# Optimization experiments

Hardware: AMD Instinct MI355X
Metric: run time of the kernel (lower is better)

Reference implementation:

```python
import jax, jax.numpy as jnp
import numpy as np

USER = 50000
ITEM = 20000
N = USER + ITEM
LATDIM = 64
GNN_LAYERS = 2
LAM = 0.2  # args.ris_adj_lambda
IMG_DIM = 4096
TXT_DIM = 768
E_MAIN = 2_000_000
E_MODAL = 1_000_000


def setup_inputs() -> dict:
    key = jax.random.key(0)
    ks = jax.random.split(key, 25)
    f32 = jnp.float32
    inp = {
        "image_embedding": jax.random.normal(ks[0], (ITEM, IMG_DIM), f32),
        "text_embedding": jax.random.normal(ks[1], (ITEM, TXT_DIM), f32),
        "adj_rows": jax.random.randint(ks[2], (E_MAIN,), 0, N, jnp.int32),
        "adj_cols": jax.random.randint(ks[3], (E_MAIN,), 0, N, jnp.int32),
        "adj_vals": jax.random.uniform(ks[4], (E_MAIN,), f32),
        "img_rows": jax.random.randint(ks[5], (E_MODAL,), 0, N, jnp.int32),
        "img_cols": jax.random.randint(ks[6], (E_MODAL,), 0, N, jnp.int32),
        "img_vals": jax.random.uniform(ks[7], (E_MODAL,), f32),
        "txt_rows": jax.random.randint(ks[8], (E_MODAL,), 0, N, jnp.int32),
        "txt_cols": jax.random.randint(ks[9], (E_MODAL,), 0, N, jnp.int32),
        "txt_vals": jax.random.uniform(ks[10], (E_MODAL,), f32),
        "u_sh": jax.random.normal(ks[11], (USER, LATDIM), f32) * 0.1,
        "i_sh": jax.random.normal(ks[12], (ITEM, LATDIM), f32) * 0.1,
        "Wi_sh": jax.random.normal(ks[13], (IMG_DIM, LATDIM), f32) * 0.02,
        "bi_sh": jnp.zeros((LATDIM,), f32),
        "Wt_sh": jax.random.normal(ks[14], (TXT_DIM, LATDIM), f32) * 0.02,
        "bt_sh": jnp.zeros((LATDIM,), f32),
        "u_vsp": jax.random.normal(ks[15], (USER, LATDIM), f32) * 0.1,
        "i_vsp": jax.random.normal(ks[16], (ITEM, LATDIM), f32) * 0.1,
        "Wi_vsp": jax.random.normal(ks[17], (IMG_DIM, LATDIM), f32) * 0.02,
        "bi_vsp": jnp.zeros((LATDIM,), f32),
        "u_tsp": jax.random.normal(ks[18], (USER, LATDIM), f32) * 0.1,
        "i_tsp": jax.random.normal(ks[19], (ITEM, LATDIM), f32) * 0.1,
        "Wt_tsp": jax.random.normal(ks[20], (TXT_DIM, LATDIM), f32) * 0.02,
        "bt_tsp": jnp.zeros((LATDIM,), f32),
    }
    return inp


def _spmm(rows, cols, vals, x):
    # sparse COO [N,N] @ dense [N,D]: gather source rows, scale, scatter-add to dest rows
    return jax.ops.segment_sum(vals[:, None] * x[cols], rows, num_segments=N)


def _l2norm(x):
    # F.normalize(x, p=2, dim=1), eps=1e-12
    n = jnp.linalg.norm(x, axis=1, keepdims=True)
    return x / jnp.maximum(n, 1e-12)


def _branch(uE, iE, feats, ar, ac, av, mr, mc, mv):
    base = jnp.concatenate([uE, iE], axis=0)
    e_adj = _spmm(mr, mc, mv, base)                                   # modal graph aggregation
    e = _spmm(ar, ac, av, jnp.concatenate([uE, _l2norm(feats)], 0))   # pass 1: normalized modal feats
    e2 = _spmm(ar, ac, av, jnp.concatenate([e[:USER], iE], 0))        # pass 2: propagated users + id emb
    e = e + e2 + LAM * e_adj
    total = e
    cur = e
    for _ in range(GNN_LAYERS):
        cur = _spmm(ar, ac, av, cur)
        total = total + cur
    return total  # [N, LATDIM]


def reference(image_embedding, text_embedding,
              adj_rows, adj_cols, adj_vals,
              img_rows, img_cols, img_vals,
              txt_rows, txt_cols, txt_vals,
              u_sh, i_sh, Wi_sh, bi_sh, Wt_sh, bt_sh,
              u_vsp, i_vsp, Wi_vsp, bi_vsp,
              u_tsp, i_tsp, Wt_tsp, bt_tsp):
    # trans == 1: Linear feature projections
    img_sh = image_embedding @ Wi_sh + bi_sh
    txt_sh = text_embedding @ Wt_sh + bt_sh
    # shared-modal model (Model_modal_sh.forward_MM)
    ev_sh = _branch(u_sh, i_sh, img_sh, adj_rows, adj_cols, adj_vals, img_rows, img_cols, img_vals)
    et_sh = _branch(u_sh, i_sh, txt_sh, adj_rows, adj_cols, adj_vals, txt_rows, txt_cols, txt_vals)
    sh = jnp.concatenate([ev_sh, et_sh], axis=-1)  # [N, 2*LATDIM]
    # visual-specific model (Model_visual_sp.forward_MM)
    img_sp = image_embedding @ Wi_vsp + bi_vsp
    ev_sp = _branch(u_vsp, i_vsp, img_sp, adj_rows, adj_cols, adj_vals, img_rows, img_cols, img_vals)
    # text-specific model (Model_text_sp.forward_MM)
    txt_sp = text_embedding @ Wt_tsp + bt_tsp
    et_sp = _branch(u_tsp, i_tsp, txt_sp, adj_rows, adj_cols, adj_vals, txt_rows, txt_cols, txt_vals)
    # pack all model outputs into one array: [N, 4*LATDIM]
    return jnp.concatenate([sh, ev_sp, et_sp], axis=-1)
```

## Files before the change

### kernel.cpp

```cpp
#include <hip/hip_runtime.h>

#define USERN 50000
#define ITEMN 20000
#define NN    70000
#define DTOT  256
#define LAMv  0.2f
#define E_MAINN  2000000
#define E_MODALN 1000000
#define SCAN_NBLK 35
#define R0BITS 4
#define NBUCK  (NN >> R0BITS)

typedef float  v4f  __attribute__((ext_vector_type(4)));
typedef float  v8f  __attribute__((ext_vector_type(8)));
typedef short  v8s  __attribute__((ext_vector_type(8)));
typedef unsigned short v8u __attribute__((ext_vector_type(8)));

__device__ inline unsigned short f2bf(float f) {
    unsigned u = __float_as_uint(f);
    u += 0x7FFFu + ((u >> 16) & 1u);
    return (unsigned short)(u >> 16);
}
__device__ inline v8f bf8f(v8u u) {
    v8f f;
    #pragma unroll
    for (int i = 0; i < 8; ++i) f[i] = __uint_as_float((unsigned)u[i] << 16);
    return f;
}
__device__ inline v8u f8bf(v8f f) {
    v8u u;
    #pragma unroll
    for (int i = 0; i < 8; ++i) u[i] = f2bf(f[i]);
    return u;
}
__device__ inline ushort4 f4bf(float4 f) {
    return make_ushort4(f2bf(f.x), f2bf(f.y), f2bf(f.z), f2bf(f.w));
}

__global__ __launch_bounds__(256) void wt_build(
    const float* __restrict__ W0, const float* __restrict__ W1, int K,
    unsigned short* __restrict__ Wtb)
{
    int idx = blockIdx.x * 256 + threadIdx.x;
    if (idx >= 128 * K) return;
    int c = idx / K, k = idx - c * K;
    float v = (c < 64) ? W0[(size_t)k * 64 + c] : W1[(size_t)k * 64 + (c - 64)];
    Wtb[idx] = f2bf(v);
}

#define LDK 40

__global__ __launch_bounds__(256) void gemm_mfma(
    const float* __restrict__ A, int M, int K,
    const unsigned short* __restrict__ Wtb,
    float* __restrict__ P, int blkA, int blkB)
{
    __shared__ __align__(16) unsigned short As[64 * LDK];
    __shared__ __align__(16) unsigned short Ws[128 * LDK];
    const int tid  = threadIdx.x;
    const int row0 = blockIdx.x * 64;
    const int segLen = K >> 1;
    const int k0   = blockIdx.y * segLen;
    const int kend = k0 + segLen;
    float* outP = P + (size_t)blockIdx.y * ITEMN * DTOT;

    const int w   = tid >> 6;
    const int l   = tid & 63;
    const int l16 = l & 15, kg = l >> 4;

    const int sar = tid >> 2, sak = (tid & 3) * 8;
    const int swc = tid >> 1, swk = (tid & 1) * 16;

    v4f acc[8];
    #pragma unroll
    for (int n = 0; n < 8; ++n) acc[n] = (v4f)0.f;

    for (int kt = k0; kt < kend; kt += 32) {
        __syncthreads();
        {
            int arow = row0 + sar; if (arow >= M) arow = M - 1;
            const float* ap = A + (size_t)arow * K + kt + sak;
            float4 a0 = ((const float4*)ap)[0];
            float4 a1 = ((const float4*)ap)[1];
            *(ushort4*)&As[sar * LDK + sak]     = f4bf(a0);
            *(ushort4*)&As[sar * LDK + sak + 4] = f4bf(a1);
            const unsigned short* wp = Wtb + (size_t)swc * K + kt + swk;
            *(uint4*)&Ws[swc * LDK + swk]     = ((const uint4*)wp)[0];
            *(uint4*)&Ws[swc * LDK + swk + 8] = ((const uint4*)wp)[1];
        }
        __syncthreads();

        v8s af = *(const v8s*)&As[(w * 16 + l16) * LDK + kg * 8];
        #pragma unroll
        for (int n = 0; n < 8; ++n) {
            v8s bf = *(const v8s*)&Ws[(n * 16 + l16) * LDK + kg * 8];
            acc[n] = __builtin_amdgcn_mfma_f32_16x16x32_bf16(af, bf, acc[n], 0, 0, 0);
        }
    }

    #pragma unroll
    for (int n = 0; n < 8; ++n) {
        const int col  = n * 16 + l16;
        const int gcol = (col < 64) ? blkA * 64 + col : blkB * 64 + (col - 64);
        #pragma unroll
        for (int r = 0; r < 4; ++r) {
            int row = row0 + w * 16 + kg * 4 + r;
            if (row < M) outP[(size_t)row * DTOT + gcol] = acc[n][r];
        }
    }
}

__global__ __launch_bounds__(256) void build_feats(
    const float* __restrict__ P,
    const float* __restrict__ u_sh, const float* __restrict__ u_vsp, const float* __restrict__ u_tsp,
    const float* __restrict__ i_sh, const float* __restrict__ i_vsp, const float* __restrict__ i_tsp,
    const float* __restrict__ bi_sh, const float* __restrict__ bt_sh,
    const float* __restrict__ bi_vsp, const float* __restrict__ bt_tsp,
    unsigned short* __restrict__ X1b, unsigned short* __restrict__ X2b)
{
    const int n = blockIdx.x;
    const int t = threadIdx.x;
    const int b = t >> 6, k = t & 63;
    if (n < USERN) {
        const float* u = (b < 2) ? u_sh : (b == 2 ? u_vsp : u_tsp);
        X1b[(size_t)n * DTOT + t] = f2bf(u[(size_t)n * 64 + k]);
    } else {
        const int it = n - USERN;
        const size_t SEG = (size_t)ITEMN * DTOT;
        size_t idx = (size_t)it * DTOT + t;
        float f = P[idx] + P[idx + SEG];
        const float* bias = (b == 0) ? bi_sh : (b == 1 ? bt_sh : (b == 2 ? bi_vsp : bt_tsp));
        f += bias[k];
        float s = f * f;
        #pragma unroll
        for (int off = 32; off > 0; off >>= 1) s += __shfl_xor(s, off, 64);
        X1b[(size_t)n * DTOT + t] = f2bf(f / fmaxf(sqrtf(s), 1e-12f));
        const float* p = (b < 2) ? i_sh : (b == 2 ? i_vsp : i_tsp);
        X2b[(size_t)n * DTOT + t] = f2bf(p[(size_t)it * 64 + k]);
    }
}

__global__ __launch_bounds__(256) void hist3(
    const int* __restrict__ ar, const int* __restrict__ mir, const int* __restrict__ mtr,
    int* __restrict__ cntA, int* __restrict__ cntI, int* __restrict__ cntT)
{
    const int total = E_MAINN + 2 * E_MODALN;
    for (int i = blockIdx.x * blockDim.x + threadIdx.x; i < total; i += gridDim.x * blockDim.x) {
        if (i < E_MAINN)                    atomicAdd(&cntA[ar[i]], 1);
        else if (i < E_MAINN + E_MODALN)    atomicAdd(&cntI[mir[i - E_MAINN]], 1);
        else                                atomicAdd(&cntT[mtr[i - E_MAINN - E_MODALN]], 1);
    }
}

__device__ inline int wave_incl_scan64(int x, int lane) {
    #pragma unroll
    for (int off = 1; off < 64; off <<= 1) {
        int t = __shfl_up(x, off, 64);
        if (lane >= off) x += t;
    }
    return x;
}

__global__ __launch_bounds__(1024) void scan_bsum(
    const int* __restrict__ cntA, const int* __restrict__ cntI, const int* __restrict__ cntT,
    int* __restrict__ partial)
{
    const int g = blockIdx.y;
    const int* cnt = (g == 0) ? cntA : (g == 1 ? cntI : cntT);
    int i0 = blockIdx.x * 2048 + threadIdx.x;
    int i1 = i0 + 1024;
    int v = ((i0 < NN) ? cnt[i0] : 0) + ((i1 < NN) ? cnt[i1] : 0);
    __shared__ int ws[16];
    const int lane = threadIdx.x & 63, wv = threadIdx.x >> 6;
    #pragma unroll
    for (int off = 32; off > 0; off >>= 1) v += __shfl_xor(v, off, 64);
    if (lane == 0) ws[wv] = v;
    __syncthreads();
    if (threadIdx.x == 0) {
        int s = 0;
        #pragma unroll
        for (int i = 0; i < 16; ++i) s += ws[i];
        partial[g * SCAN_NBLK + blockIdx.x] = s;
    }
}

__global__ __launch_bounds__(1024) void scan_write(
    const int* __restrict__ cntA, const int* __restrict__ cntI, const int* __restrict__ cntT,
    const int* __restrict__ partial,
    int* __restrict__ rpA, int* __restrict__ rpI, int* __restrict__ rpT)
{
    const int g = blockIdx.y;
    const int* cnt = (g == 0) ? cntA : (g == 1 ? cntI : cntT);
    int* rp        = (g == 0) ? rpA  : (g == 1 ? rpI  : rpT);
    __shared__ int sbase;
    __shared__ int wsum[16];
    const int tid = threadIdx.x, lane = tid & 63, wv = tid >> 6;
    if (tid == 0) {
        int s = 0;
        for (int i = 0; i < (int)blockIdx.x; ++i) s += partial[g * SCAN_NBLK + i];
        sbase = s;
    }
    __syncthreads();
    int run = sbase;
    const int base = blockIdx.x * 2048;
    #pragma unroll
    for (int c = 0; c < 2; ++c) {
        int i = base + c * 1024 + tid;
        int v = (i < NN) ? cnt[i] : 0;
        int x = wave_incl_scan64(v, lane);
        if (lane == 63) wsum[wv] = x;
        __syncthreads();
        if (wv == 0 && lane < 16) {
            int s = wsum[lane];
            #pragma unroll
            for (int off = 1; off < 16; off <<= 1) {
                int t = __shfl_up(s, off, 64);
                if (lane >= off) s += t;
            }
            wsum[lane] = s;
        }
        __syncthreads();
        int woff = (wv > 0) ? wsum[wv - 1] : 0;
        if (i < NN)       rp[i]  = run + woff + x - v;
        else if (i == NN) rp[NN] = run + woff + x;
        run += wsum[15];
        __syncthreads();
    }
}

__global__ __launch_bounds__(256) void partition3(
    const int* __restrict__ ar,  const int* __restrict__ ac,  const float* __restrict__ av,
    const int* __restrict__ mir, const int* __restrict__ mic, const float* __restrict__ miv,
    const int* __restrict__ mtr, const int* __restrict__ mtc, const float* __restrict__ mtv,
    const int* __restrict__ rpA, const int* __restrict__ rpI, const int* __restrict__ rpT,
    int* __restrict__ bcnt,
    uint2* __restrict__ tmpA, uint2* __restrict__ tmpI, uint2* __restrict__ tmpT)
{
    const int total = E_MAINN + 2 * E_MODALN;
    for (int i = blockIdx.x * blockDim.x + threadIdx.x; i < total; i += gridDim.x * blockDim.x) {
        if (i < E_MAINN) {
            int r = ar[i], b = r >> R0BITS;
            int pos = rpA[b << R0BITS] + atomicAdd(&bcnt[b], 1);
            tmpA[pos] = make_uint2(((unsigned)(r & 15) << 17) | (unsigned)ac[i], __float_as_uint(av[i]));
        } else if (i < E_MAINN + E_MODALN) {
            int e = i - E_MAINN;
            int r = mir[e], b = r >> R0BITS;
            int pos = rpI[b << R0BITS] + atomicAdd(&bcnt[NBUCK + b], 1);
            tmpI[pos] = make_uint2(((unsigned)(r & 15) << 17) | (unsigned)mic[e], __float_as_uint(miv[e]));
        } else {
            int e = i - E_MAINN - E_MODALN;
            int r = mtr[e], b = r >> R0BITS;
            int pos = rpT[b << R0BITS] + atomicAdd(&bcnt[2 * NBUCK + b], 1);
            tmpT[pos] = make_uint2(((unsigned)(r & 15) << 17) | (unsigned)mtc[e], __float_as_uint(mtv[e]));
        }
    }
}

__global__ __launch_bounds__(256) void local_scatter(
    const int* __restrict__ rpA, const int* __restrict__ rpI, const int* __restrict__ rpT,
    const uint2* __restrict__ tmpA, const uint2* __restrict__ tmpI, const uint2* __restrict__ tmpT,
    uint2* __restrict__ evA, uint2* __restrict__ evI, uint2* __restrict__ evT)
{
    const int g = blockIdx.y;
    const int* rp     = (g == 0) ? rpA  : (g == 1 ? rpI  : rpT);
    const uint2* tmp  = (g == 0) ? tmpA : (g == 1 ? tmpI : tmpT);
    uint2* ev         = (g == 0) ? evA  : (g == 1 ? evI  : evT);
    const int r0 = blockIdx.x << R0BITS;
    __shared__ int lrp[17];
    __shared__ int lcnt[16];
    const int tid = threadIdx.x;
    if (tid < 17) lrp[tid] = rp[r0 + tid];
    if (tid < 16) lcnt[tid] = 0;
    __syncthreads();
    const int base = lrp[0];
    const int count = lrp[16] - base;
    for (int t = tid; t < count; t += 256) {
        uint2 q = tmp[base + t];
        int rl = q.x >> 17;
        int k = atomicAdd(&lcnt[rl], 1);
        ev[lrp[rl] + k] = make_uint2(q.x & 0x1FFFFu, q.y);
    }
}

#define SPMM8_HEAD                                                                  \
    const int w = (blockIdx.x * blockDim.x + threadIdx.x) >> 6;                     \
    if (w >= NN) return;                                                            \
    const int lane = threadIdx.x & 63;                                              \
    const int half = lane >> 5, l5 = lane & 31;                                     \
    const v8u* __restrict__ Xv = (const v8u*)Xb;                                    \
    int e = rp[w]; const int end = rp[w + 1];                                       \
    v8f acc = (v8f)0.f;                                                             \
    for (; e + 8 <= end; e += 8) {                                                  \
        uint2 q0 = ev[e + half],     q1 = ev[e + 2 + half];                         \
        uint2 q2 = ev[e + 4 + half], q3 = ev[e + 6 + half];                         \
        v8f g0 = bf8f(Xv[(size_t)q0.x * 32 + l5]);                                  \
        v8f g1 = bf8f(Xv[(size_t)q1.x * 32 + l5]);                                  \
        v8f g2 = bf8f(Xv[(size_t)q2.x * 32 + l5]);                                  \
        v8f g3 = bf8f(Xv[(size_t)q3.x * 32 + l5]);                                  \
        float v0 = __uint_as_float(q0.y), v1 = __uint_as_float(q1.y);               \
        float v2 = __uint_as_float(q2.y), v3 = __uint_as_float(q3.y);               \
        _Pragma("unroll")                                                           \
        for (int i = 0; i < 8; ++i) {                                               \
            acc[i] = fmaf(v0, g0[i], acc[i]); acc[i] = fmaf(v1, g1[i], acc[i]);     \
            acc[i] = fmaf(v2, g2[i], acc[i]); acc[i] = fmaf(v3, g3[i], acc[i]);     \
        }                                                                           \
    }                                                                               \
    for (; e + 2 <= end; e += 2) {                                                  \
        uint2 q = ev[e + half];                                                     \
        v8f g = bf8f(Xv[(size_t)q.x * 32 + l5]);                                    \
        float v = __uint_as_float(q.y);                                             \
        _Pragma("unroll")                                                           \
        for (int i = 0; i < 8; ++i) acc[i] = fmaf(v, g[i], acc[i]);                 \
    }                                                                               \
    if (e < end && half == 0) {                                                     \
        uint2 q = ev[e];                                                            \
        v8f g = bf8f(Xv[(size_t)q.x * 32 + l5]);                                    \
        float v = __uint_as_float(q.y);                                             \
        _Pragma("unroll")                                                           \
        for (int i = 0; i < 8; ++i) acc[i] = fmaf(v, g[i], acc[i]);                 \
    }                                                                               \
    _Pragma("unroll")                                                               \
    for (int i = 0; i < 8; ++i) acc[i] += __shfl_xor(acc[i], 32, 64);               \
    if (half != 0) return;                                                          \
    const size_t oidx = (size_t)w * DTOT + l5 * 8;

__global__ __launch_bounds__(256) void spmm_e1(
    const int* __restrict__ rp, const uint2* __restrict__ ev,
    const unsigned short* __restrict__ Xb, unsigned short* __restrict__ E1b,
    unsigned short* __restrict__ X2b)
{
    SPMM8_HEAD
    v8u ub = f8bf(acc);
    *(v8u*)&E1b[oidx] = ub;
    if (w < USERN) *(v8u*)&X2b[oidx] = ub;
}

__global__ __launch_bounds__(256) void fused_comb_main(
    const int* __restrict__ rp, const uint2* __restrict__ ev,
    const unsigned short* __restrict__ Xb, const unsigned short* __restrict__ E1b,
    float* __restrict__ out)
{
    SPMM8_HEAD
    v8f o = bf8f(*(const v8u*)&E1b[oidx]);
    #pragma unroll
    for (int i = 0; i < 8; ++i) o[i] += acc[i];
    *(v8f*)&out[oidx] = o;
}

__global__ __launch_bounds__(256) void spmm_l1(
    const int* __restrict__ rp, const uint2* __restrict__ ev,
    const unsigned short* __restrict__ Xb, unsigned short* __restrict__ C1b)
{
    SPMM8_HEAD
    *(v8u*)&C1b[oidx] = f8bf(acc);
}

__global__ __launch_bounds__(256) void fused_final(
    const int* __restrict__ rp, const uint2* __restrict__ ev,
    const unsigned short* __restrict__ Xb, float* __restrict__ out)
{
    SPMM8_HEAD
    v8f o = *(const v8f*)&out[oidx];
    v8f c = bf8f(Xv[(size_t)w * 32 + l5]);
    #pragma unroll
    for (int i = 0; i < 8; ++i) o[i] += c[i] + acc[i];
    *(v8f*)&out[oidx] = o;
}

__global__ __launch_bounds__(256) void modal_add(
    const int* __restrict__ rpI, const uint2* __restrict__ evI,
    const int* __restrict__ rpT, const uint2* __restrict__ evT,
    const unsigned short* __restrict__ X1b, const unsigned short* __restrict__ X2b,
    float* __restrict__ out, unsigned short* __restrict__ OUTb)
{
    const int gw = (blockIdx.x * blockDim.x + threadIdx.x) >> 6;
    if (gw >= 2 * NN) return;
    const int r = gw >> 1, m = gw & 1;
    const int lane = threadIdx.x & 63;
    const int qt = lane >> 4, l4 = lane & 15;
    const int* rp   = m ? rpT : rpI;
    const uint2* ev = m ? evT : evI;
    const int slot = m * 8 + (l4 >> 3) * 16 + (l4 & 7);
    const v8u* X1v = (const v8u*)X1b;
    const v8u* X2v = (const v8u*)X2b;
    v8f acc = (v8f)0.f;
    int e = rp[r]; const int end = rp[r + 1];
    for (; e + 4 <= end; e += 4) {
        uint2 q = ev[e + qt];
        const v8u* B = ((int)q.x < USERN) ? X1v : X2v;
        v8f g = bf8f(B[(size_t)q.x * 32 + slot]);
        float v = __uint_as_float(q.y) * LAMv;
        #pragma unroll
        for (int i = 0; i < 8; ++i) acc[i] = fmaf(v, g[i], acc[i]);
    }
    if (qt < end - e) {
        uint2 q = ev[e + qt];
        const v8u* B = ((int)q.x < USERN) ? X1v : X2v;
        v8f g = bf8f(B[(size_t)q.x * 32 + slot]);
        float v = __uint_as_float(q.y) * LAMv;
        #pragma unroll
        for (int i = 0; i < 8; ++i) acc[i] = fmaf(v, g[i], acc[i]);
    }
    #pragma unroll
    for (int i = 0; i < 8; ++i) {
        acc[i] += __shfl_xor(acc[i], 16, 64);
        acc[i] += __shfl_xor(acc[i], 32, 64);
    }
    if (lane < 16) {
        const size_t idx = (size_t)r * DTOT + slot * 8;
        v8f o = *(const v8f*)&out[idx];
        #pragma unroll
        for (int i = 0; i < 8; ++i) o[i] += acc[i];
        *(v8f*)&out[idx] = o;
        *(v8u*)&OUTb[idx] = f8bf(o);
    }
}

extern "C" void kernel_launch(void* const* d_in, const int* in_sizes, int n_in,
                              void* d_out, int out_size, void* d_ws, size_t ws_size,
                              hipStream_t stream)
{
    const float* img = (const float*)d_in[0];
    const float* txt = (const float*)d_in[1];
    const int*   ar  = (const int*)d_in[2];
    const int*   ac  = (const int*)d_in[3];
    const float* av  = (const float*)d_in[4];
    const int*   mir = (const int*)d_in[5];
    const int*   mic = (const int*)d_in[6];
    const float* miv = (const float*)d_in[7];
    const int*   mtr = (const int*)d_in[8];
    const int*   mtc = (const int*)d_in[9];
    const float* mtv = (const float*)d_in[10];
    const float* u_sh   = (const float*)d_in[11];
    const float* i_sh   = (const float*)d_in[12];
    const float* Wi_sh  = (const float*)d_in[13];
    const float* bi_sh  = (const float*)d_in[14];
    const float* Wt_sh  = (const float*)d_in[15];
    const float* bt_sh  = (const float*)d_in[16];
    const float* u_vsp  = (const float*)d_in[17];
    const float* i_vsp  = (const float*)d_in[18];
    const float* Wi_vsp = (const float*)d_in[19];
    const float* bi_vsp = (const float*)d_in[20];
    const float* u_tsp  = (const float*)d_in[21];
    const float* i_tsp  = (const float*)d_in[22];
    const float* Wt_tsp = (const float*)d_in[23];
    const float* bt_tsp = (const float*)d_in[24];

    const size_t NE = (size_t)NN * DTOT;
    unsigned short* X1b  = (unsigned short*)d_ws;
    unsigned short* X2b  = X1b + NE;
    unsigned short* OUTb = X2b + NE;
    unsigned short* E1b  = OUTb + NE;
    unsigned short* C1b  = X1b;
    float* P = (float*)(E1b + NE);
    unsigned short* WtbI = (unsigned short*)(P + 2 * (size_t)ITEMN * DTOT);
    unsigned short* WtbT = WtbI + 128 * 4096;
    uint2* evA  = (uint2*)(WtbT + 128 * 768);
    uint2* evI  = evA + E_MAINN;
    uint2* evT  = evI + E_MODALN;
    uint2* tmpA = evT + E_MODALN;
    uint2* tmpI = tmpA + E_MAINN;
    uint2* tmpT = tmpI + E_MODALN;
    int*   rpA   = (int*)(tmpT + E_MODALN);
    int*   rpI   = rpA + (NN + 4);
    int*   rpT   = rpI + (NN + 4);
    int*   cntA  = rpT + (NN + 4);
    int*   cntI  = cntA + NN;
    int*   cntT  = cntI + NN;
    int*   bcnt  = cntT + NN;
    int*   partial = bcnt + 3 * NBUCK;
    float* out   = (float*)d_out;

    const int waveBlocks  = (NN * 64) / 256;
    const int modalBlocks = (2 * NN * 64) / 256;

    hipMemsetAsync(cntA, 0, (3 * (size_t)NN + 3 * NBUCK) * sizeof(int), stream);
    hist3<<<2048, 256, 0, stream>>>(ar, mir, mtr, cntA, cntI, cntT);
    scan_bsum<<<dim3(SCAN_NBLK, 3), 1024, 0, stream>>>(cntA, cntI, cntT, partial);
    scan_write<<<dim3(SCAN_NBLK, 3), 1024, 0, stream>>>(cntA, cntI, cntT, partial, rpA, rpI, rpT);
    partition3<<<2048, 256, 0, stream>>>(ar, ac, av, mir, mic, miv, mtr, mtc, mtv,
                                         rpA, rpI, rpT, bcnt, tmpA, tmpI, tmpT);
    local_scatter<<<dim3(NBUCK, 3), 256, 0, stream>>>(rpA, rpI, rpT, tmpA, tmpI, tmpT, evA, evI, evT);

    wt_build<<<(128 * 4096 + 255) / 256, 256, 0, stream>>>(Wi_sh, Wi_vsp, 4096, WtbI);
    wt_build<<<(128 * 768  + 255) / 256, 256, 0, stream>>>(Wt_sh, Wt_tsp,  768, WtbT);

    gemm_mfma<<<dim3((ITEMN + 63) / 64, 2), 256, 0, stream>>>(img, ITEMN, 4096, WtbI, P, 0, 2);
    gemm_mfma<<<dim3((ITEMN + 63) / 64, 2), 256, 0, stream>>>(txt, ITEMN,  768, WtbT, P, 1, 3);

    build_feats<<<NN, 256, 0, stream>>>(P, u_sh, u_vsp, u_tsp, i_sh, i_vsp, i_tsp,
                                        bi_sh, bt_sh, bi_vsp, bt_tsp, X1b, X2b);

    spmm_e1<<<waveBlocks, 256, 0, stream>>>(rpA, evA, X1b, E1b, X2b);

    fused_comb_main<<<waveBlocks, 256, 0, stream>>>(rpA, evA, X2b, E1b, out);

    modal_add<<<modalBlocks, 256, 0, stream>>>(rpI, evI, rpT, evT, X1b, X2b, out, OUTb);

    spmm_l1<<<waveBlocks, 256, 0, stream>>>(rpA, evA, OUTb, C1b);

    fused_final<<<waveBlocks, 256, 0, stream>>>(rpA, evA, C1b, out);
}
```

Measured before the change: 1.272 ms.

## Replace atomic-histogram CSR build with two-pass bucketed radix partition

Builds the three CSR structures with a coarse pass that splits rows into 64 buckets, staging edges in shared memory and flushing them in chunks, followed by a per-bucket local sort that computes row pointers in LDS. This replaces the per-row global atomic histogram, the multi-block scan, and the global-atomic partition, aiming to cut global atomic traffic and scattered writes. The cost is that the second pass runs only 64 blocks per graph, each handling about 30K edges, so parallelism is low. Shared-memory overflow falls back to global atomics.

Result: faster. 1.133 ms (-11.0%).

```diff
diff --git a/kernel.cpp b/kernel.cpp
--- a/kernel.cpp
+++ b/kernel.cpp
@@ -7,9 +7,12 @@
 #define LAMv  0.2f
 #define E_MAINN  2000000
 #define E_MODALN 1000000
-#define SCAN_NBLK 35
-#define R0BITS 4
-#define NBUCK  (NN >> R0BITS)
+#define B1    64
+#define RPB1  1094
+#define CAP   96
+#define FLUSH 64
+#define NBLK1 128
+#define SPAN  5
 
 typedef float  v4f  __attribute__((ext_vector_type(4)));
 typedef float  v8f  __attribute__((ext_vector_type(8)));
@@ -35,6 +38,15 @@
 }
 __device__ inline ushort4 f4bf(float4 f) {
     return make_ushort4(f2bf(f.x), f2bf(f.y), f2bf(f.z), f2bf(f.w));
+}
+
+__device__ inline int wave_incl_scan64(int x, int lane) {
+    #pragma unroll
+    for (int off = 1; off < 64; off <<= 1) {
+        int t = __shfl_up(x, off, 64);
+        if (lane >= off) x += t;
+    }
+    return x;
 }
 
 __global__ __launch_bounds__(256) void wt_build(
@@ -140,145 +152,162 @@
     }
 }
 
-__global__ __launch_bounds__(256) void hist3(
+__global__ __launch_bounds__(256) void bucket_count(
     const int* __restrict__ ar, const int* __restrict__ mir, const int* __restrict__ mtr,
-    int* __restrict__ cntA, int* __restrict__ cntI, int* __restrict__ cntT)
-{
-    const int total = E_MAINN + 2 * E_MODALN;
-    for (int i = blockIdx.x * blockDim.x + threadIdx.x; i < total; i += gridDim.x * blockDim.x) {
-        if (i < E_MAINN)                    atomicAdd(&cntA[ar[i]], 1);
-        else if (i < E_MAINN + E_MODALN)    atomicAdd(&cntI[mir[i - E_MAINN]], 1);
-        else                                atomicAdd(&cntT[mtr[i - E_MAINN - E_MODALN]], 1);
-    }
-}
-
-__device__ inline int wave_incl_scan64(int x, int lane) {
-    #pragma unroll
-    for (int off = 1; off < 64; off <<= 1) {
-        int t = __shfl_up(x, off, 64);
-        if (lane >= off) x += t;
-    }
-    return x;
-}
-
-__global__ __launch_bounds__(1024) void scan_bsum(
-    const int* __restrict__ cntA, const int* __restrict__ cntI, const int* __restrict__ cntT,
-    int* __restrict__ partial)
+    int* __restrict__ bcount)
 {
     const int g = blockIdx.y;
-    const int* cnt = (g == 0) ? cntA : (g == 1 ? cntI : cntT);
-    int i0 = blockIdx.x * 2048 + threadIdx.x;
-    int i1 = i0 + 1024;
-    int v = ((i0 < NN) ? cnt[i0] : 0) + ((i1 < NN) ? cnt[i1] : 0);
-    __shared__ int ws[16];
-    const int lane = threadIdx.x & 63, wv = threadIdx.x >> 6;
-    #pragma unroll
-    for (int off = 32; off > 0; off >>= 1) v += __shfl_xor(v, off, 64);
-    if (lane == 0) ws[wv] = v;
-    __syncthreads();
-    if (threadIdx.x == 0) {
-        int s = 0;
-        #pragma unroll
-        for (int i = 0; i < 16; ++i) s += ws[i];
-        partial[g * SCAN_NBLK + blockIdx.x] = s;
-    }
-}
-
-__global__ __launch_bounds__(1024) void scan_write(
-    const int* __restrict__ cntA, const int* __restrict__ cntI, const int* __restrict__ cntT,
-    const int* __restrict__ partial,
-    int* __restrict__ rpA, int* __restrict__ rpI, int* __restrict__ rpT)
-{
-    const int g = blockIdx.y;
-    const int* cnt = (g == 0) ? cntA : (g == 1 ? cntI : cntT);
-    int* rp        = (g == 0) ? rpA  : (g == 1 ? rpI  : rpT);
-    __shared__ int sbase;
-    __shared__ int wsum[16];
-    const int tid = threadIdx.x, lane = tid & 63, wv = tid >> 6;
-    if (tid == 0) {
-        int s = 0;
-        for (int i = 0; i < (int)blockIdx.x; ++i) s += partial[g * SCAN_NBLK + i];
-        sbase = s;
-    }
-    __syncthreads();
-    int run = sbase;
-    const int base = blockIdx.x * 2048;
-    #pragma unroll
-    for (int c = 0; c < 2; ++c) {
-        int i = base + c * 1024 + tid;
-        int v = (i < NN) ? cnt[i] : 0;
+    const int* rows = (g == 0) ? ar : (g == 1 ? mir : mtr);
+    const int E = (g == 0) ? E_MAINN : E_MODALN;
+    __shared__ int h[B1];
+    if (threadIdx.x < B1) h[threadIdx.x] = 0;
+    __syncthreads();
+    const int chunk = (E + gridDim.x - 1) / gridDim.x;
+    const int c0 = blockIdx.x * chunk, c1 = min(c0 + chunk, E);
+    for (int i = c0 + threadIdx.x; i < c1; i += 256)
+        atomicAdd(&h[rows[i] / RPB1], 1);
+    __syncthreads();
+    if (threadIdx.x < B1 && h[threadIdx.x])
+        atomicAdd(&bcount[g * B1 + threadIdx.x], h[threadIdx.x]);
+}
+
+__global__ __launch_bounds__(256) void bucket_base(
+    const int* __restrict__ bcount, int* __restrict__ gbase, int* __restrict__ gcnt)
+{
+    const int g = threadIdx.x >> 6, lane = threadIdx.x & 63;
+    if (g < 3) {
+        int v = bcount[g * B1 + lane];
         int x = wave_incl_scan64(v, lane);
-        if (lane == 63) wsum[wv] = x;
-        __syncthreads();
-        if (wv == 0 && lane < 16) {
-            int s = wsum[lane];
-            #pragma unroll
-            for (int off = 1; off < 16; off <<= 1) {
-                int t = __shfl_up(s, off, 64);
-                if (lane >= off) s += t;
-            }
-            wsum[lane] = s;
-        }
-        __syncthreads();
-        int woff = (wv > 0) ? wsum[wv - 1] : 0;
-        if (i < NN)       rp[i]  = run + woff + x - v;
-        else if (i == NN) rp[NN] = run + woff + x;
-        run += wsum[15];
-        __syncthreads();
-    }
-}
-
-__global__ __launch_bounds__(256) void partition3(
+        gbase[g * (B1 + 1) + lane] = x - v;
+        if (lane == 63) gbase[g * (B1 + 1) + B1] = x;
+        gcnt[g * B1 + lane] = 0;
+    }
+}
+
+__global__ __launch_bounds__(256) void radix_a(
     const int* __restrict__ ar,  const int* __restrict__ ac,  const float* __restrict__ av,
     const int* __restrict__ mir, const int* __restrict__ mic, const float* __restrict__ miv,
     const int* __restrict__ mtr, const int* __restrict__ mtc, const float* __restrict__ mtv,
-    const int* __restrict__ rpA, const int* __restrict__ rpI, const int* __restrict__ rpT,
-    int* __restrict__ bcnt,
+    const int* __restrict__ gbase, int* __restrict__ gcnt,
     uint2* __restrict__ tmpA, uint2* __restrict__ tmpI, uint2* __restrict__ tmpT)
 {
-    const int total = E_MAINN + 2 * E_MODALN;
-    for (int i = blockIdx.x * blockDim.x + threadIdx.x; i < total; i += gridDim.x * blockDim.x) {
-        if (i < E_MAINN) {
-            int r = ar[i], b = r >> R0BITS;
-            int pos = rpA[b << R0BITS] + atomicAdd(&bcnt[b], 1);
-            tmpA[pos] = make_uint2(((unsigned)(r & 15) << 17) | (unsigned)ac[i], __float_as_uint(av[i]));
-        } else if (i < E_MAINN + E_MODALN) {
-            int e = i - E_MAINN;
-            int r = mir[e], b = r >> R0BITS;
-            int pos = rpI[b << R0BITS] + atomicAdd(&bcnt[NBUCK + b], 1);
-            tmpI[pos] = make_uint2(((unsigned)(r & 15) << 17) | (unsigned)mic[e], __float_as_uint(miv[e]));
-        } else {
-            int e = i - E_MAINN - E_MODALN;
-            int r = mtr[e], b = r >> R0BITS;
-            int pos = rpT[b << R0BITS] + atomicAdd(&bcnt[2 * NBUCK + b], 1);
-            tmpT[pos] = make_uint2(((unsigned)(r & 15) << 17) | (unsigned)mtc[e], __float_as_uint(mtv[e]));
+    const int g = blockIdx.y;
+    const int* rows   = (g == 0) ? ar : (g == 1 ? mir : mtr);
+    const int* cols   = (g == 0) ? ac : (g == 1 ? mic : mtc);
+    const float* vals = (g == 0) ? av : (g == 1 ? miv : mtv);
+    uint2* tmp        = (g == 0) ? tmpA : (g == 1 ? tmpI : tmpT);
+    const int E = (g == 0) ? E_MAINN : E_MODALN;
+    const int* gb = gbase + g * (B1 + 1);
+    int* gc = gcnt + g * B1;
+
+    __shared__ uint2 buf[B1][CAP];
+    __shared__ int bcnt_s[B1];
+    const int tid = threadIdx.x;
+    if (tid < B1) bcnt_s[tid] = 0;
+    __syncthreads();
+
+    const int chunk = (E + gridDim.x - 1) / gridDim.x;
+    const int c0 = blockIdx.x * chunk, c1 = min(c0 + chunk, E);
+    const int b = tid >> 2, sub = tid & 3;
+    const int blane = (tid & 63) & ~3;
+
+    for (int base = c0; base < c1; base += 256) {
+        int i = base + tid;
+        if (i < c1) {
+            int r = rows[i];
+            int b1 = r / RPB1;
+            int rl = r - b1 * RPB1;
+            uint2 entry = make_uint2(((unsigned)rl << 17) | (unsigned)cols[i],
+                                     __float_as_uint(vals[i]));
+            int slot = atomicAdd(&bcnt_s[b1], 1);
+            if (slot < CAP) buf[b1][slot] = entry;
+            else tmp[gb[b1] + atomicAdd(&gc[b1], 1)] = entry;
         }
-    }
-}
-
-__global__ __launch_bounds__(256) void local_scatter(
-    const int* __restrict__ rpA, const int* __restrict__ rpI, const int* __restrict__ rpT,
-    const uint2* __restrict__ tmpA, const uint2* __restrict__ tmpI, const uint2* __restrict__ tmpT,
-    uint2* __restrict__ evA, uint2* __restrict__ evI, uint2* __restrict__ evT)
-{
-    const int g = blockIdx.y;
-    const int* rp     = (g == 0) ? rpA  : (g == 1 ? rpI  : rpT);
-    const uint2* tmp  = (g == 0) ? tmpA : (g == 1 ? tmpI : tmpT);
-    uint2* ev         = (g == 0) ? evA  : (g == 1 ? evI  : evT);
-    const int r0 = blockIdx.x << R0BITS;
-    __shared__ int lrp[17];
-    __shared__ int lcnt[16];
-    const int tid = threadIdx.x;
-    if (tid < 17) lrp[tid] = rp[r0 + tid];
-    if (tid < 16) lcnt[tid] = 0;
-    __syncthreads();
-    const int base = lrp[0];
-    const int count = lrp[16] - base;
-    for (int t = tid; t < count; t += 256) {
-        uint2 q = tmp[base + t];
-        int rl = q.x >> 17;
-        int k = atomicAdd(&lcnt[rl], 1);
-        ev[lrp[rl] + k] = make_uint2(q.x & 0x1FFFFu, q.y);
+        __syncthreads();
+        int bc = min(bcnt_s[b], CAP);
+        if (bc >= FLUSH) {
+            int goff = 0;
+            if (sub == 0) goff = gb[b] + atomicAdd(&gc[b], FLUSH);
+            goff = __shfl(goff, blane, 64);
+            for (int t = sub; t < FLUSH; t += 4)
+                tmp[goff + t] = buf[b][t];
+            int rem = bc - FLUSH;
+            for (int t = sub; t < rem; t += 4)
+                buf[b][t] = buf[b][FLUSH + t];
+            if (sub == 0) bcnt_s[b] = rem;
+        }
+        __syncthreads();
+    }
+    int bc = min(bcnt_s[b], CAP);
+    if (bc > 0) {
+        int goff = 0;
+        if (sub == 0) goff = gb[b] + atomicAdd(&gc[b], bc);
+        goff = __shfl(goff, blane, 64);
+        for (int t = sub; t < bc; t += 4)
+            tmp[goff + t] = buf[b][t];
+    }
+}
+
+__global__ __launch_bounds__(256) void bucket_sort(
+    const int* __restrict__ gbase,
+    const uint2* __restrict__ tmp, uint2* __restrict__ ev, int* __restrict__ rp, int gidx)
+{
+    const int b1 = blockIdx.x;
+    const int r0 = b1 * RPB1;
+    const int r1 = min(r0 + RPB1, NN);
+    const int nr = r1 - r0;
+    const int gb = gbase[gidx * (B1 + 1) + b1];
+    const int count = gbase[gidx * (B1 + 1) + b1 + 1] - gb;
+    __shared__ int lcnt[RPB1];
+    __shared__ int lrp[RPB1];
+    __shared__ int wsum[4];
+    const int tid = threadIdx.x, lane = tid & 63, wv = tid >> 6;
+    for (int t = tid; t < nr; t += 256) lcnt[t] = 0;
+    __syncthreads();
+    for (int t = tid; t < count; t += 256)
+        atomicAdd(&lcnt[tmp[gb + t].x >> 17], 1);
+    __syncthreads();
+    int loc[SPAN]; int s = 0;
+    #pragma unroll
+    for (int j = 0; j < SPAN; ++j) {
+        int idx = tid * SPAN + j;
+        int v = (idx < nr) ? lcnt[idx] : 0;
+        loc[j] = s; s += v;
+    }
+    int x = wave_incl_scan64(s, lane);
+    if (lane == 63) wsum[wv] = x;
+    __syncthreads();
+    int woff = 0;
+    for (int i = 0; i < wv; ++i) woff += wsum[i];
+    int ex = woff + x - s;
+    #pragma unroll
+    for (int j = 0; j < SPAN; ++j) {
+        int idx = tid * SPAN + j;
+        if (idx < nr) lrp[idx] = gb + ex + loc[j];
+    }
+    __syncthreads();
+    for (int t = tid; t < nr; t += 256) rp[r0 + t] = lrp[t];
+    if (tid == 0 && r1 == NN) rp[NN] = gb + count;
+    __syncthreads();
+    int t = tid;
+    for (; t + 768 < count; t += 1024) {
+        uint2 q0 = tmp[gb + t];
+        uint2 q1 = tmp[gb + t + 256];
+        uint2 q2 = tmp[gb + t + 512];
+        uint2 q3 = tmp[gb + t + 768];
+        int p0 = atomicAdd(&lrp[q0.x >> 17], 1);
+        int p1 = atomicAdd(&lrp[q1.x >> 17], 1);
+        int p2 = atomicAdd(&lrp[q2.x >> 17], 1);
+        int p3 = atomicAdd(&lrp[q3.x >> 17], 1);
+        ev[p0] = make_uint2(q0.x & 0x1FFFFu, q0.y);
+        ev[p1] = make_uint2(q1.x & 0x1FFFFu, q1.y);
+        ev[p2] = make_uint2(q2.x & 0x1FFFFu, q2.y);
+        ev[p3] = make_uint2(q3.x & 0x1FFFFu, q3.y);
+    }
+    for (; t < count; t += 256) {
+        uint2 q = tmp[gb + t];
+        int p = atomicAdd(&lrp[q.x >> 17], 1);
+        ev[p] = make_uint2(q.x & 0x1FFFFu, q.y);
     }
 }
 
@@ -464,23 +493,22 @@
     int*   rpA   = (int*)(tmpT + E_MODALN);
     int*   rpI   = rpA + (NN + 4);
     int*   rpT   = rpI + (NN + 4);
-    int*   cntA  = rpT + (NN + 4);
-    int*   cntI  = cntA + NN;
-    int*   cntT  = cntI + NN;
-    int*   bcnt  = cntT + NN;
-    int*   partial = bcnt + 3 * NBUCK;
+    int*   bcount = rpT + (NN + 4);
+    int*   gbase  = bcount + 3 * B1;
+    int*   gcnt   = gbase + 3 * (B1 + 1);
     float* out   = (float*)d_out;
 
     const int waveBlocks  = (NN * 64) / 256;
     const int modalBlocks = (2 * NN * 64) / 256;
 
-    hipMemsetAsync(cntA, 0, (3 * (size_t)NN + 3 * NBUCK) * sizeof(int), stream);
-    hist3<<<2048, 256, 0, stream>>>(ar, mir, mtr, cntA, cntI, cntT);
-    scan_bsum<<<dim3(SCAN_NBLK, 3), 1024, 0, stream>>>(cntA, cntI, cntT, partial);
-    scan_write<<<dim3(SCAN_NBLK, 3), 1024, 0, stream>>>(cntA, cntI, cntT, partial, rpA, rpI, rpT);
-    partition3<<<2048, 256, 0, stream>>>(ar, ac, av, mir, mic, miv, mtr, mtc, mtv,
-                                         rpA, rpI, rpT, bcnt, tmpA, tmpI, tmpT);
-    local_scatter<<<dim3(NBUCK, 3), 256, 0, stream>>>(rpA, rpI, rpT, tmpA, tmpI, tmpT, evA, evI, evT);
+    hipMemsetAsync(bcount, 0, 3 * B1 * sizeof(int), stream);
+    bucket_count<<<dim3(NBLK1, 3), 256, 0, stream>>>(ar, mir, mtr, bcount);
+    bucket_base<<<1, 256, 0, stream>>>(bcount, gbase, gcnt);
+    radix_a<<<dim3(NBLK1, 3), 256, 0, stream>>>(ar, ac, av, mir, mic, miv, mtr, mtc, mtv,
+                                                gbase, gcnt, tmpA, tmpI, tmpT);
+    bucket_sort<<<B1, 256, 0, stream>>>(gbase, tmpA, evA, rpA, 0);
+    bucket_sort<<<B1, 256, 0, stream>>>(gbase, tmpI, evI, rpI, 1);
+    bucket_sort<<<B1, 256, 0, stream>>>(gbase, tmpT, evT, rpT, 2);
 
     wt_build<<<(128 * 4096 + 255) / 256, 256, 0, stream>>>(Wi_sh, Wi_vsp, 4096, WtbI);
     wt_build<<<(128 * 768  + 255) / 256, 256, 0, stream>>>(Wt_sh, Wt_tsp,  768, WtbT);
```
